# Kernel tuning notes

Hardware: AMD Instinct MI355X
Metric: run time of the kernel (lower is better)

## Reference

```python
import jax, jax.numpy as jnp
import numpy as np

EMBED_DIM = 1024
NUM_HEADS = 16
HEAD_DIM = EMBED_DIM // NUM_HEADS
EPS = 1e-5


def setup_inputs() -> dict:
    key = jax.random.key(0)
    ks = jax.random.split(key, 7)
    B, S, D = 4, 2048, EMBED_DIM
    s = 1.0 / np.sqrt(D)
    return {
        "x": jax.random.normal(ks[0], (B, S, D), dtype=jnp.float32),
        "W_qkv": jax.random.uniform(ks[1], (D, 3 * D), jnp.float32, -s, s),
        "b_qkv": jax.random.uniform(ks[2], (3 * D,), jnp.float32, -s, s),
        "W_out": jax.random.uniform(ks[3], (D, D), jnp.float32, -s, s),
        "b_out": jax.random.uniform(ks[4], (D,), jnp.float32, -s, s),
        "gamma": jnp.ones((D,), jnp.float32),
        "beta": jnp.zeros((D,), jnp.float32),
    }


def _layer_norm(y, gamma, beta):
    mu = jnp.mean(y, axis=-1, keepdims=True)
    var = jnp.mean(jnp.square(y - mu), axis=-1, keepdims=True)
    return (y - mu) * jax.lax.rsqrt(var + EPS) * gamma + beta


def reference(x, W_qkv, b_qkv, W_out, b_out, gamma, beta):
    B, S, D = x.shape
    H, Hd = NUM_HEADS, HEAD_DIM
    qkv = x @ W_qkv + b_qkv                       # [B,S,3D]
    q, k, v = jnp.split(qkv, 3, axis=-1)
    q = q.reshape(B, S, H, Hd).transpose(0, 2, 1, 3)  # [B,H,S,Hd]
    k = k.reshape(B, S, H, Hd).transpose(0, 2, 1, 3)
    v = v.reshape(B, S, H, Hd).transpose(0, 2, 1, 3)
    scale = 1.0 / np.sqrt(Hd)
    scores = jnp.einsum("bhsd,bhtd->bhst", q, k) * scale  # [B,H,S,S]
    attn = jax.nn.softmax(scores, axis=-1)
    ctx = jnp.einsum("bhst,bhtd->bhsd", attn, v)  # [B,H,S,Hd]
    ctx = ctx.transpose(0, 2, 1, 3).reshape(B, S, D)
    out = ctx @ W_out + b_out
    return _layer_norm(out + x, gamma, beta)
```

## Files before the change

### kernel.cpp

```cpp
#include <hip/hip_runtime.h>
#include <stdint.h>
#include <stddef.h>


#define SEQ    2048
#define DMODEL 1024
#define NHEAD  16
#define HDIM   64

typedef __attribute__((ext_vector_type(4))) float f32x4;
typedef __attribute__((ext_vector_type(16))) float f32x16;
typedef __attribute__((ext_vector_type(8))) short bf16x8;
typedef __attribute__((ext_vector_type(2))) unsigned uint2v;

static __device__ __forceinline__ unsigned short f2b(float f) {
  union { float f; unsigned u; } c; c.f = f;
  unsigned r = c.u + 0x7FFFu + ((c.u >> 16) & 1u);
  return (unsigned short)(r >> 16);
}
static __device__ __forceinline__ unsigned pkbf(float lo, float hi_) {
  unsigned r;
  asm("v_cvt_pk_bf16_f32 %0, %1, %2" : "=v"(r) : "v"(lo), "v"(hi_));
  return r;
}
static __device__ __forceinline__ float exp2v(float x) {
  return __builtin_amdgcn_exp2f(x);
}
static __device__ __forceinline__ uint2v swap32(unsigned a, unsigned b) {
  return __builtin_amdgcn_permlane32_swap(a, b, false, false);
}
static __device__ __forceinline__ void gl_lds16(const void* g, void* l) {
  __builtin_amdgcn_global_load_lds((const __attribute__((address_space(1))) void*)g,
                                   (__attribute__((address_space(3))) void*)l, 16, 0, 0);
}
static __device__ __forceinline__ int swz(int row, int col) {
  return (row * 64 + col) ^ ((row & 7) << 3);
}

__global__ __launch_bounds__(256) void k_cvt(const float* __restrict__ in,
                                             unsigned short* __restrict__ out) {
  const size_t i = ((size_t)blockIdx.x * 256 + threadIdx.x) * 8;
  f32x4 a = *(const f32x4*)&in[i];
  f32x4 b = *(const f32x4*)&in[i + 4];
  bf16x8 o;
  o[0] = (short)f2b(a[0]); o[1] = (short)f2b(a[1]);
  o[2] = (short)f2b(a[2]); o[3] = (short)f2b(a[3]);
  o[4] = (short)f2b(b[0]); o[5] = (short)f2b(b[1]);
  o[6] = (short)f2b(b[2]); o[7] = (short)f2b(b[3]);
  *(bf16x8*)&out[i] = o;
}

__global__ __launch_bounds__(256) void k_transpose_cvt(const float* __restrict__ in,
                                                       unsigned short* __restrict__ out,
                                                       int R, int C) {
  __shared__ unsigned short tile[32][33];
  const int c0 = blockIdx.x * 32, r0 = blockIdx.y * 32;
  const int tx = threadIdx.x, ty = threadIdx.y;
#pragma unroll
  for (int j = 0; j < 4; j++) {
    int rr = ty + j * 8;
    tile[rr][tx] = f2b(in[(size_t)(r0 + rr) * C + c0 + tx]);
  }
  __syncthreads();
#pragma unroll
  for (int j = 0; j < 4; j++) {
    int rr = ty + j * 8;
    out[(size_t)(c0 + rr) * R + r0 + tx] = tile[tx][rr];
  }
}

__global__ __launch_bounds__(256) void k_gemm_qkv(const unsigned short* __restrict__ X,
                                                  const unsigned short* __restrict__ WT,
                                                  const float* __restrict__ bias,
                                                  unsigned short* __restrict__ qb,
                                                  unsigned short* __restrict__ kb,
                                                  unsigned short* __restrict__ vt) {
  __shared__ __align__(16) unsigned short As[128 * 32];
  __shared__ __align__(16) unsigned short Bs[128 * 32];
  const int t = threadIdx.x;
  const int w = t >> 6, l = t & 63, g = l >> 4, r = l & 15;
  const int wr = w >> 1, wc = w & 1;
  const int bm = blockIdx.x * 128;
  const int bn = blockIdx.y * 128;

  f32x4 acc[4][4];
#pragma unroll
  for (int a = 0; a < 4; a++)
#pragma unroll
    for (int b = 0; b < 4; b++) acc[a][b] = f32x4{0.f, 0.f, 0.f, 0.f};

  for (int k0 = 0; k0 < DMODEL; k0 += 32) {
    __syncthreads();
#pragma unroll
    for (int j = 0; j < 2; j++) {
      int idx = t + j * 256;
      int row = idx >> 2, kc = idx & 3;
      gl_lds16(X + (size_t)(bm + row) * DMODEL + k0 + kc * 8, (char*)As + idx * 16);
      gl_lds16(WT + (size_t)(bn + row) * DMODEL + k0 + kc * 8, (char*)Bs + idx * 16);
    }
    __syncthreads();
    bf16x8 af[4], bf[4];
#pragma unroll
    for (int mf = 0; mf < 4; mf++)
      af[mf] = *(const bf16x8*)&As[(wr * 64 + mf * 16 + r) * 32 + g * 8];
#pragma unroll
    for (int nf = 0; nf < 4; nf++)
      bf[nf] = *(const bf16x8*)&Bs[(wc * 64 + nf * 16 + r) * 32 + g * 8];
#pragma unroll
    for (int mf = 0; mf < 4; mf++)
#pragma unroll
      for (int nf = 0; nf < 4; nf++)
        acc[mf][nf] = __builtin_amdgcn_mfma_f32_16x16x32_bf16(af[mf], bf[nf], acc[mf][nf], 0, 0, 0);
  }

  if (blockIdx.y >= 16) {
    __syncthreads();
    const int bi = bm >> 11, sbase = bm & 2047;
    const int h  = ((bn - 2048) >> 6) + wc;
    const int bh = bi * NHEAD + h;
    unsigned short* Ls = (w < 2) ? (As + w * 2048) : (Bs + (w - 2) * 2048);
#pragma unroll
    for (int p = 0; p < 2; p++) {
#pragma unroll
      for (int nfp = 0; nfp < 2; nfp++)
#pragma unroll
        for (int mf = 0; mf < 4; mf++)
#pragma unroll
          for (int i = 0; i < 4; i++) {
            const int nf = 2 * p + nfp;
            const int dd = nfp * 16 + r;
            const int ss = mf * 16 + g * 4 + i;
            float v = acc[mf][nf][i] + bias[bn + wc * 64 + nf * 16 + r];
            Ls[dd * 64 + (((ss >> 3) ^ (dd & 7)) * 8) + (ss & 7)] = f2b(v);
          }
#pragma unroll
      for (int j = 0; j < 4; j++) {
        const int dd = l >> 1;
        const int ch = (l & 1) * 4 + j;
        bf16x8 ov = *(const bf16x8*)&Ls[dd * 64 + ((ch ^ (dd & 7)) * 8)];
        *(bf16x8*)&vt[((size_t)bh * HDIM + 32 * p + dd) * SEQ + sbase + wr * 64 + ch * 8] = ov;
      }
    }
  } else {
#pragma unroll
    for (int mf = 0; mf < 4; mf++)
#pragma unroll
      for (int nf = 0; nf < 4; nf++)
#pragma unroll
        for (int i = 0; i < 4; i++) {
          int m = bm + wr * 64 + mf * 16 + g * 4 + i;
          int n = bn + wc * 64 + nf * 16 + r;
          float v = acc[mf][nf][i] + bias[n];
          int part = n >> 10, rem = n & 1023, h = rem >> 6, d = rem & 63;
          int bi = m >> 11, s = m & 2047;
          int bh = bi * NHEAD + h;
          if (part == 0)      qb[((size_t)bh * SEQ + s) * HDIM + d] = f2b(v * 0.18033688f);
          else                kb[((size_t)bh * SEQ + s) * HDIM + d] = f2b(v);
        }
  }
}

__global__ __launch_bounds__(256) void k_attn(const unsigned short* __restrict__ qb,
                                              const unsigned short* __restrict__ kb,
                                              const unsigned short* __restrict__ vt,
                                              unsigned short* __restrict__ ctx) {
  __shared__ __align__(16) unsigned short Qs[128 * 64];
  __shared__ __align__(16) unsigned short K0[64 * 64];
  __shared__ __align__(16) unsigned short V0[64 * 64];
  const int t = threadIdx.x;
  const int w = t >> 6, l = t & 63;
  const int ql = l & 31, hi = l >> 5;
  const int q0 = blockIdx.x * 128;
  const int bh = blockIdx.y;
  const size_t qoff = ((size_t)bh * SEQ + q0) * HDIM;

#pragma unroll
  for (int j = 0; j < 4; j++) {
    int idx = t + j * 256;
    int row = idx >> 3, s = idx & 7;
    gl_lds16(qb + qoff + (size_t)row * 64 + (s ^ (row & 7)) * 8, (char*)Qs + idx * 16);
  }
#pragma unroll
  for (int j = 0; j < 2; j++) {
    int idx = t + j * 256;
    int row = idx >> 3, s = idx & 7;
    gl_lds16(kb + ((size_t)bh * SEQ + row) * HDIM + (s ^ (row & 7)) * 8, (char*)K0 + idx * 16);
    gl_lds16(vt + ((size_t)bh * HDIM + row) * SEQ + (s ^ (row & 7)) * 8, (char*)V0 + idx * 16);
  }
  asm volatile("s_waitcnt vmcnt(4)" ::: "memory");
  __builtin_amdgcn_sched_barrier(0);
  __builtin_amdgcn_s_barrier();

  bf16x8 qf[4];
#pragma unroll
  for (int ds = 0; ds < 4; ds++)
    qf[ds] = *(const bf16x8*)&Qs[swz(w * 32 + ql, ds * 16 + hi * 8)];
  asm volatile("s_waitcnt lgkmcnt(0)" ::: "memory");
  __builtin_amdgcn_sched_barrier(0);
  __builtin_amdgcn_s_barrier();

  bf16x8 ones;
#pragma unroll
  for (int i = 0; i < 8; i++) ones[i] = (short)0x3F80;

  f32x16 acc_o[2];
  f32x16 acc_l;
#pragma unroll
  for (int db = 0; db < 2; db++)
#pragma unroll
    for (int i = 0; i < 16; i++) acc_o[db][i] = 0.f;
#pragma unroll
  for (int i = 0; i < 16; i++) acc_l[i] = 0.f;

  for (int it = 0; it < SEQ / 64; ++it) {
    const int b = it & 1;
    if (it + 1 < SEQ / 64) {
      const int kt = (it + 1) * 64;
      unsigned short* Kd = (b ^ 1) ? Qs : K0;
      unsigned short* Vd = (b ^ 1) ? (Qs + 4096) : V0;
#pragma unroll
      for (int j = 0; j < 2; j++) {
        int idx = t + j * 256;
        int row = idx >> 3, s = idx & 7;
        gl_lds16(kb + ((size_t)bh * SEQ + kt + row) * HDIM + (s ^ (row & 7)) * 8,
                 (char*)Kd + idx * 16);
        gl_lds16(vt + ((size_t)bh * HDIM + row) * SEQ + kt + (s ^ (row & 7)) * 8,
                 (char*)Vd + idx * 16);
      }
      asm volatile("s_waitcnt vmcnt(4)" ::: "memory");
    } else {
      asm volatile("s_waitcnt vmcnt(0)" ::: "memory");
    }
    __builtin_amdgcn_sched_barrier(0);
    __builtin_amdgcn_s_barrier();

    const unsigned short* Kb = b ? Qs : K0;
    const unsigned short* Vb = b ? (Qs + 4096) : V0;

    bf16x8 kf[2][4];
#pragma unroll
    for (int kb2 = 0; kb2 < 2; kb2++)
#pragma unroll
      for (int ds = 0; ds < 4; ds++)
        kf[kb2][ds] = *(const bf16x8*)&Kb[swz(kb2 * 32 + ql, ds * 16 + hi * 8)];

    f32x16 accs[2];
#pragma unroll
    for (int kb2 = 0; kb2 < 2; kb2++)
#pragma unroll
      for (int i = 0; i < 16; i++) accs[kb2][i] = 0.f;
    __builtin_amdgcn_s_setprio(1);
#pragma unroll
    for (int ds = 0; ds < 4; ds++)
#pragma unroll
      for (int kb2 = 0; kb2 < 2; kb2++)
        accs[kb2] = __builtin_amdgcn_mfma_f32_32x32x16_bf16(kf[kb2][ds], qf[ds], accs[kb2], 0, 0, 0);
    __builtin_amdgcn_s_setprio(0);

#pragma unroll
    for (int kb2 = 0; kb2 < 2; kb2++)
#pragma unroll
      for (int i = 0; i < 16; i++) accs[kb2][i] = exp2v(accs[kb2][i]);

    bf16x8 pa[4];
#pragma unroll
    for (int ks = 0; ks < 4; ks++) {
      const int kb2 = ks >> 1, rb = (ks & 1) * 8;
      unsigned wA0 = pkbf(accs[kb2][rb + 0], accs[kb2][rb + 1]);
      unsigned wA1 = pkbf(accs[kb2][rb + 2], accs[kb2][rb + 3]);
      unsigned wB0 = pkbf(accs[kb2][rb + 4], accs[kb2][rb + 5]);
      unsigned wB1 = pkbf(accs[kb2][rb + 6], accs[kb2][rb + 7]);
      uint2v s0 = swap32(wB0, wA0);
      uint2v s1 = swap32(wB1, wA1);
      union { bf16x8 v; unsigned u[4]; } fr;
      fr.u[0] = s0[1]; fr.u[1] = s1[1]; fr.u[2] = s0[0]; fr.u[3] = s1[0];
      pa[ks] = fr.v;
    }

    bf16x8 vf[2][4];
#pragma unroll
    for (int db = 0; db < 2; db++)
#pragma unroll
      for (int ks = 0; ks < 4; ks++)
        vf[db][ks] = *(const bf16x8*)&Vb[swz(db * 32 + ql, ks * 16 + hi * 8)];

    __builtin_amdgcn_s_setprio(1);
#pragma unroll
    for (int ks = 0; ks < 4; ks++) {
#pragma unroll
      for (int db = 0; db < 2; db++)
        acc_o[db] = __builtin_amdgcn_mfma_f32_32x32x16_bf16(vf[db][ks], pa[ks], acc_o[db], 0, 0, 0);
      acc_l = __builtin_amdgcn_mfma_f32_32x32x16_bf16(ones, pa[ks], acc_l, 0, 0, 0);
    }
    __builtin_amdgcn_s_setprio(0);

    __builtin_amdgcn_s_barrier();
  }

  const int bi = bh >> 4, h = bh & 15;
  const float rl = 1.f / acc_l[0];
  unsigned short* Ls = Qs + w * 2048;
#pragma unroll
  for (int db = 0; db < 2; db++)
#pragma unroll
    for (int j = 0; j < 8; j++) {
      const int d0 = db * 32 + (j & 1) * 2 + (j >> 1) * 8 + hi * 4;
      *(unsigned*)&Ls[(ql * 64 + d0) ^ ((ql & 7) << 3)] =
          pkbf(acc_o[db][2 * j] * rl, acc_o[db][2 * j + 1] * rl);
    }
#pragma unroll
  for (int rq = 0; rq < 4; rq++) {
    const int q = rq * 8 + (l >> 3);
    const int c8 = l & 7;
    bf16x8 ov = *(const bf16x8*)&Ls[(q * 64 + c8 * 8) ^ ((q & 7) << 3)];
    *(bf16x8*)&ctx[((size_t)bi * SEQ + q0 + w * 32 + q) * DMODEL + h * 64 + c8 * 8] = ov;
  }
}

__global__ __launch_bounds__(256) void k_gemm_out(const unsigned short* __restrict__ A,
                                                  const unsigned short* __restrict__ WT,
                                                  const float* __restrict__ bias,
                                                  const float* __restrict__ X,
                                                  float* __restrict__ Y) {
  __shared__ __align__(16) unsigned short As[128 * 32];
  __shared__ __align__(16) unsigned short Bs[128 * 32];
  const int t = threadIdx.x;
  const int w = t >> 6, l = t & 63, g = l >> 4, r = l & 15;
  const int wr = w >> 1, wc = w & 1;
  const int bm = blockIdx.x * 128;
  const int bn = blockIdx.y * 128;

  f32x4 acc[4][4];
#pragma unroll
  for (int a = 0; a < 4; a++)
#pragma unroll
    for (int b = 0; b < 4; b++) acc[a][b] = f32x4{0.f, 0.f, 0.f, 0.f};

  for (int k0 = 0; k0 < DMODEL; k0 += 32) {
    __syncthreads();
#pragma unroll
    for (int j = 0; j < 2; j++) {
      int idx = t + j * 256;
      int row = idx >> 2, kc = idx & 3;
      gl_lds16(A + (size_t)(bm + row) * DMODEL + k0 + kc * 8, (char*)As + idx * 16);
      gl_lds16(WT + (size_t)(bn + row) * DMODEL + k0 + kc * 8, (char*)Bs + idx * 16);
    }
    __syncthreads();
    bf16x8 af[4], bf[4];
#pragma unroll
    for (int mf = 0; mf < 4; mf++)
      af[mf] = *(const bf16x8*)&As[(wr * 64 + mf * 16 + r) * 32 + g * 8];
#pragma unroll
    for (int nf = 0; nf < 4; nf++)
      bf[nf] = *(const bf16x8*)&Bs[(wc * 64 + nf * 16 + r) * 32 + g * 8];
#pragma unroll
    for (int mf = 0; mf < 4; mf++)
#pragma unroll
      for (int nf = 0; nf < 4; nf++)
        acc[mf][nf] = __builtin_amdgcn_mfma_f32_16x16x32_bf16(af[mf], bf[nf], acc[mf][nf], 0, 0, 0);
  }

#pragma unroll
  for (int mf = 0; mf < 4; mf++)
#pragma unroll
    for (int nf = 0; nf < 4; nf++)
#pragma unroll
      for (int i = 0; i < 4; i++) {
        int m = bm + wr * 64 + mf * 16 + g * 4 + i;
        int n = bn + wc * 64 + nf * 16 + r;
        float v = acc[mf][nf][i] + bias[n] + X[(size_t)m * DMODEL + n];
        Y[(size_t)m * DMODEL + n] = v;
      }
}

__global__ __launch_bounds__(256) void k_ln(const float* __restrict__ Y,
                                            const float* __restrict__ gamma,
                                            const float* __restrict__ beta,
                                            float* __restrict__ out) {
  const int row = blockIdx.x, t = threadIdx.x;
  const float* y = Y + (size_t)row * DMODEL;
  f32x4 v = *(const f32x4*)&y[t * 4];
  float s = v[0] + v[1] + v[2] + v[3];
  float q = v[0] * v[0] + v[1] * v[1] + v[2] * v[2] + v[3] * v[3];
#pragma unroll
  for (int m = 1; m < 64; m <<= 1) { s += __shfl_xor(s, m); q += __shfl_xor(q, m); }
  __shared__ float ss[4], sq[4];
  const int w = t >> 6, l = t & 63;
  if (l == 0) { ss[w] = s; sq[w] = q; }
  __syncthreads();
  s = ss[0] + ss[1] + ss[2] + ss[3];
  q = sq[0] + sq[1] + sq[2] + sq[3];
  const float mu = s * (1.f / DMODEL);
  const float var = q * (1.f / DMODEL) - mu * mu;
  const float rs = rsqrtf(var + 1e-5f);
  f32x4 o;
#pragma unroll
  for (int j = 0; j < 4; j++)
    o[j] = (v[j] - mu) * rs * gamma[t * 4 + j] + beta[t * 4 + j];
  *(f32x4*)&out[(size_t)row * DMODEL + t * 4] = o;
}

extern "C" void kernel_launch(void* const* d_in, const int* in_sizes, int n_in,
                              void* d_out, int out_size, void* d_ws, size_t ws_size,
                              hipStream_t stream) {
  const float* X     = (const float*)d_in[0];
  const float* Wqkv  = (const float*)d_in[1];
  const float* bqkv  = (const float*)d_in[2];
  const float* Wout  = (const float*)d_in[3];
  const float* bout  = (const float*)d_in[4];
  const float* gamma = (const float*)d_in[5];
  const float* beta  = (const float*)d_in[6];

  char* ws = (char*)d_ws;
  unsigned short* wqkvT = (unsigned short*)(ws);
  unsigned short* woutT = (unsigned short*)(ws + 6291456);
  unsigned short* Xb    = (unsigned short*)(ws + 8388608);
  unsigned short* ctx   = (unsigned short*)(ws + 8388608);
  unsigned short* qb    = (unsigned short*)(ws + 25165824);
  unsigned short* kb    = (unsigned short*)(ws + 41943040);
  unsigned short* vt    = (unsigned short*)(ws + 58720256);
  float*          Yf    = (float*)d_out;

  dim3 tb(32, 8, 1);
  k_transpose_cvt<<<dim3(96, 32, 1), tb, 0, stream>>>(Wqkv, wqkvT, 1024, 3072);
  k_transpose_cvt<<<dim3(32, 32, 1), tb, 0, stream>>>(Wout, woutT, 1024, 1024);
  k_cvt<<<dim3(4096, 1, 1), dim3(256, 1, 1), 0, stream>>>(X, Xb);
  k_gemm_qkv<<<dim3(64, 24, 1), dim3(256, 1, 1), 0, stream>>>(Xb, wqkvT, bqkv, qb, kb, vt);
  k_attn<<<dim3(16, 64, 1), dim3(256, 1, 1), 0, stream>>>(qb, kb, vt, ctx);
  k_gemm_out<<<dim3(64, 8, 1), dim3(256, 1, 1), 0, stream>>>(ctx, woutT, bout, X, Yf);
  k_ln<<<dim3(8192, 1, 1), dim3(256, 1, 1), 0, stream>>>(Yf, gamma, beta, (float*)d_out);
}
```

Measured before the change: 228.7 us.

## Merge prep kernels into one launch and load V fragments directly from global

Combines the two weight transpose-convert launches and the activation convert launch into a single k_prep kernel that picks its role from the block index, removing two launches. In the attention kernel, V tiles are no longer staged through LDS with async global-to-LDS copies. Each lane now reads its V fragments directly from global memory into registers, which frees one LDS buffer and cuts LDS traffic. The cost is that these global loads are synchronous in the inner loop and may expose latency on the PV MFMAs.

Result: slower. 260.7 us (+14.0%).

```diff
diff --git a/kernel.cpp b/kernel.cpp
--- a/kernel.cpp
+++ b/kernel.cpp
@@ -37,35 +37,43 @@
   return (row * 64 + col) ^ ((row & 7) << 3);
 }
 
-__global__ __launch_bounds__(256) void k_cvt(const float* __restrict__ in,
-                                             unsigned short* __restrict__ out) {
-  const size_t i = ((size_t)blockIdx.x * 256 + threadIdx.x) * 8;
-  f32x4 a = *(const f32x4*)&in[i];
-  f32x4 b = *(const f32x4*)&in[i + 4];
-  bf16x8 o;
-  o[0] = (short)f2b(a[0]); o[1] = (short)f2b(a[1]);
-  o[2] = (short)f2b(a[2]); o[3] = (short)f2b(a[3]);
-  o[4] = (short)f2b(b[0]); o[5] = (short)f2b(b[1]);
-  o[6] = (short)f2b(b[2]); o[7] = (short)f2b(b[3]);
-  *(bf16x8*)&out[i] = o;
-}
-
-__global__ __launch_bounds__(256) void k_transpose_cvt(const float* __restrict__ in,
-                                                       unsigned short* __restrict__ out,
-                                                       int R, int C) {
+__global__ __launch_bounds__(256) void k_prep(const float* __restrict__ Wqkv,
+                                              const float* __restrict__ Wout,
+                                              const float* __restrict__ X,
+                                              unsigned short* __restrict__ wqkvT,
+                                              unsigned short* __restrict__ woutT,
+                                              unsigned short* __restrict__ Xb) {
   __shared__ unsigned short tile[32][33];
-  const int c0 = blockIdx.x * 32, r0 = blockIdx.y * 32;
-  const int tx = threadIdx.x, ty = threadIdx.y;
-#pragma unroll
-  for (int j = 0; j < 4; j++) {
-    int rr = ty + j * 8;
-    tile[rr][tx] = f2b(in[(size_t)(r0 + rr) * C + c0 + tx]);
-  }
-  __syncthreads();
-#pragma unroll
-  for (int j = 0; j < 4; j++) {
-    int rr = ty + j * 8;
-    out[(size_t)(c0 + rr) * R + r0 + tx] = tile[tx][rr];
+  const int bid = blockIdx.x;
+  const int t = threadIdx.x;
+  if (bid < 4096) {
+    const float* in; unsigned short* out; int C, bx, by;
+    if (bid < 3072) { in = Wqkv; out = wqkvT; C = 3072; bx = bid % 96; by = bid / 96; }
+    else { int b2 = bid - 3072; in = Wout; out = woutT; C = 1024; bx = b2 & 31; by = b2 >> 5; }
+    const int R = 1024;
+    const int c0 = bx * 32, r0 = by * 32;
+    const int tx = t & 31, ty = t >> 5;
+#pragma unroll
+    for (int j = 0; j < 4; j++) {
+      int rr = ty + j * 8;
+      tile[rr][tx] = f2b(in[(size_t)(r0 + rr) * C + c0 + tx]);
+    }
+    __syncthreads();
+#pragma unroll
+    for (int j = 0; j < 4; j++) {
+      int rr = ty + j * 8;
+      out[(size_t)(c0 + rr) * R + r0 + tx] = tile[tx][rr];
+    }
+  } else {
+    const size_t i = ((size_t)(bid - 4096) * 256 + t) * 8;
+    f32x4 a = *(const f32x4*)&X[i];
+    f32x4 b = *(const f32x4*)&X[i + 4];
+    bf16x8 o;
+    o[0] = (short)f2b(a[0]); o[1] = (short)f2b(a[1]);
+    o[2] = (short)f2b(a[2]); o[3] = (short)f2b(a[3]);
+    o[4] = (short)f2b(b[0]); o[5] = (short)f2b(b[1]);
+    o[6] = (short)f2b(b[2]); o[7] = (short)f2b(b[3]);
+    *(bf16x8*)&Xb[i] = o;
   }
 }
 
@@ -166,7 +174,6 @@
                                               unsigned short* __restrict__ ctx) {
   __shared__ __align__(16) unsigned short Qs[128 * 64];
   __shared__ __align__(16) unsigned short K0[64 * 64];
-  __shared__ __align__(16) unsigned short V0[64 * 64];
   const int t = threadIdx.x;
   const int w = t >> 6, l = t & 63;
   const int ql = l & 31, hi = l >> 5;
@@ -185,9 +192,8 @@
     int idx = t + j * 256;
     int row = idx >> 3, s = idx & 7;
     gl_lds16(kb + ((size_t)bh * SEQ + row) * HDIM + (s ^ (row & 7)) * 8, (char*)K0 + idx * 16);
-    gl_lds16(vt + ((size_t)bh * HDIM + row) * SEQ + (s ^ (row & 7)) * 8, (char*)V0 + idx * 16);
-  }
-  asm volatile("s_waitcnt vmcnt(4)" ::: "memory");
+  }
+  asm volatile("s_waitcnt vmcnt(2)" ::: "memory");
   __builtin_amdgcn_sched_barrier(0);
   __builtin_amdgcn_s_barrier();
 
@@ -199,6 +205,9 @@
   __builtin_amdgcn_sched_barrier(0);
   __builtin_amdgcn_s_barrier();
 
+  const unsigned short* vp0 = vt + ((size_t)bh * HDIM + ql) * SEQ + hi * 8;
+  const unsigned short* vp1 = vp0 + (size_t)32 * SEQ;
+
   bf16x8 ones;
 #pragma unroll
   for (int i = 0; i < 8; i++) ones[i] = (short)0x3F80;
@@ -217,17 +226,14 @@
     if (it + 1 < SEQ / 64) {
       const int kt = (it + 1) * 64;
       unsigned short* Kd = (b ^ 1) ? Qs : K0;
-      unsigned short* Vd = (b ^ 1) ? (Qs + 4096) : V0;
 #pragma unroll
       for (int j = 0; j < 2; j++) {
         int idx = t + j * 256;
         int row = idx >> 3, s = idx & 7;
         gl_lds16(kb + ((size_t)bh * SEQ + kt + row) * HDIM + (s ^ (row & 7)) * 8,
                  (char*)Kd + idx * 16);
-        gl_lds16(vt + ((size_t)bh * HDIM + row) * SEQ + kt + (s ^ (row & 7)) * 8,
-                 (char*)Vd + idx * 16);
       }
-      asm volatile("s_waitcnt vmcnt(4)" ::: "memory");
+      asm volatile("s_waitcnt vmcnt(2)" ::: "memory");
     } else {
       asm volatile("s_waitcnt vmcnt(0)" ::: "memory");
     }
@@ -235,7 +241,6 @@
     __builtin_amdgcn_s_barrier();
 
     const unsigned short* Kb = b ? Qs : K0;
-    const unsigned short* Vb = b ? (Qs + 4096) : V0;
 
     bf16x8 kf[2][4];
 #pragma unroll
@@ -279,10 +284,11 @@
 
     bf16x8 vf[2][4];
 #pragma unroll
-    for (int db = 0; db < 2; db++)
-#pragma unroll
-      for (int ks = 0; ks < 4; ks++)
-        vf[db][ks] = *(const bf16x8*)&Vb[swz(db * 32 + ql, ks * 16 + hi * 8)];
+    for (int ks = 0; ks < 4; ks++) {
+      vf[0][ks] = *(const bf16x8*)(vp0 + ks * 16);
+      vf[1][ks] = *(const bf16x8*)(vp1 + ks * 16);
+    }
+    vp0 += 64; vp1 += 64;
 
     __builtin_amdgcn_s_setprio(1);
 #pragma unroll
@@ -421,10 +427,7 @@
   unsigned short* vt    = (unsigned short*)(ws + 58720256);
   float*          Yf    = (float*)d_out;
 
-  dim3 tb(32, 8, 1);
-  k_transpose_cvt<<<dim3(96, 32, 1), tb, 0, stream>>>(Wqkv, wqkvT, 1024, 3072);
-  k_transpose_cvt<<<dim3(32, 32, 1), tb, 0, stream>>>(Wout, woutT, 1024, 1024);
-  k_cvt<<<dim3(4096, 1, 1), dim3(256, 1, 1), 0, stream>>>(X, Xb);
+  k_prep<<<dim3(8192, 1, 1), dim3(256, 1, 1), 0, stream>>>(Wqkv, Wout, X, wqkvT, woutT, Xb);
   k_gemm_qkv<<<dim3(64, 24, 1), dim3(256, 1, 1), 0, stream>>>(Xb, wqkvT, bqkv, qb, kb, vt);
   k_attn<<<dim3(16, 64, 1), dim3(256, 1, 1), 0, stream>>>(qb, kb, vt, ctx);
   k_gemm_out<<<dim3(64, 8, 1), dim3(256, 1, 1), 0, stream>>>(ctx, woutT, bout, X, Yf);
```
